# Optimization experiments

Measured on AMD Instinct MI355X. Metric: run time of the kernel, lower is better.

## Reference

```python
import jax, jax.numpy as jnp
import numpy as np

D_MODEL = 512
N_HEADS = 8
D_HEAD = D_MODEL // N_HEADS
MAX_LEN = 5000


def _make_pe():
    # sinusoidal table for relative positions -MAX_LEN..+MAX_LEN
    pos = np.arange(-MAX_LEN, MAX_LEN + 1, dtype=np.float32)[:, None]
    div = np.exp(np.arange(0, D_MODEL, 2, dtype=np.float32) * (-np.log(10000.0) / D_MODEL))
    pe = np.zeros((2 * MAX_LEN + 1, D_MODEL), dtype=np.float32)
    pe[:, 0::2] = np.sin(pos * div)
    pe[:, 1::2] = np.cos(pos * div)
    return jnp.asarray(pe)


def setup_inputs() -> dict:
    key = jax.random.key(0)
    ks = jax.random.split(key, 10)
    B, S = 8, 512
    xavier = lambda k: jax.random.uniform(k, (D_MODEL, D_MODEL), jnp.float32,
                                          -np.sqrt(6.0 / (2 * D_MODEL)), np.sqrt(6.0 / (2 * D_MODEL)))
    return {
        "x": jax.random.normal(ks[0], (B, S, D_MODEL), jnp.float32),
        "wq": xavier(ks[1]), "bq": jnp.zeros((D_MODEL,), jnp.float32),
        "wk": xavier(ks[2]), "bk": jnp.zeros((D_MODEL,), jnp.float32),
        "wv": xavier(ks[3]), "bv": jnp.zeros((D_MODEL,), jnp.float32),
        "wo": xavier(ks[4]), "bo": jnp.zeros((D_MODEL,), jnp.float32),
        "wr": xavier(ks[5]),
        "u": jnp.zeros((N_HEADS, D_HEAD), jnp.float32),
        "v_bias": jnp.zeros((N_HEADS, D_HEAD), jnp.float32),
        "pe": _make_pe(),
    }


def reference(x, wq, bq, wk, bk, wv, bv, wo, bo, wr, u, v_bias, pe):
    B, S, D = x.shape
    H, dh = N_HEADS, D_HEAD
    scale = dh ** -0.5

    # projections (torch Linear: x @ W.T + b) -> [B, H, S, dh]
    def proj(w, b):
        return (x @ w.T + b).reshape(B, S, H, dh).transpose(0, 2, 1, 3)
    q = proj(wq, bq)
    k = proj(wk, bk)
    v = proj(wv, bv)

    # relative position encodings: rel[i,j] = pe[clip(j-i) + MAX_LEN]
    pos = jnp.arange(S)
    rel_idx = jnp.clip(pos[None, :] - pos[:, None], -MAX_LEN, MAX_LEN) + MAX_LEN
    rel_pos = pe[rel_idx]                              # [S, S, D]
    rel_proj = (rel_pos @ wr.T).reshape(S, S, H, dh)   # [S, S, H, dh]
    rel_proj = rel_proj.transpose(2, 0, 1, 3)          # [H, S, S, dh]

    content = jnp.einsum('bhid,bhjd->bhij', q + u[None, :, None, :], k)
    position = jnp.einsum('bhid,hijd->bhij', q + v_bias[None, :, None, :], rel_proj)
    attn = jax.nn.softmax((content + position) * scale, axis=-1)

    out = jnp.einsum('bhij,bhjd->bhid', attn, v)       # [B, H, S, dh]
    out = out.transpose(0, 2, 1, 3).reshape(B, S, D)
    return out @ wo.T + bo
```

## Files before the change

### kernel.cpp

```cpp
#include <hip/hip_runtime.h>
#include <math.h>

#define DM 512
#define NH 8
#define DH 64
#define SEQ 512
#define BATCH 8
#define MR 1023
#define PE_OFF 4489

typedef float4 f4;
typedef __attribute__((ext_vector_type(8))) short bf16x8;
typedef __attribute__((ext_vector_type(4))) float f32x4;
typedef __attribute__((ext_vector_type(8))) unsigned short u16x8;
typedef __attribute__((ext_vector_type(4))) unsigned short u16x4;

__device__ __forceinline__ unsigned short f2bf(float f) {
    unsigned x = __float_as_uint(f);
    unsigned r = x + 0x7fffu + ((x >> 16) & 1u);
    return (unsigned short)(r >> 16);
}
__device__ __forceinline__ float bf2f(unsigned short h) {
    return __uint_as_float(((unsigned)h) << 16);
}
__device__ __forceinline__ f32x4 mfma16(bf16x8 a, bf16x8 b, f32x4 c) {
    return __builtin_amdgcn_mfma_f32_16x16x32_bf16(a, b, c, 0, 0, 0);
}
__device__ __forceinline__ void gll16(const unsigned short* g, unsigned short* l) {
    __builtin_amdgcn_global_load_lds(
        (const __attribute__((address_space(1))) unsigned int*)g,
        (__attribute__((address_space(3))) unsigned int*)l, 16, 0, 0);
}

__device__ __forceinline__ void cvt8s(const float* __restrict__ src,
                                      unsigned short* __restrict__ hi,
                                      unsigned short* __restrict__ lo, int i) {
    const int row = i >> 9, col = i & 511;
    const int j = (i & ~511) | (col ^ (((row >> 1) & 3) << 3));
    f4 a = *(const f4*)&src[i];
    f4 b = *(const f4*)&src[i + 4];
    float v[8] = {a.x, a.y, a.z, a.w, b.x, b.y, b.z, b.w};
    u16x8 h, l;
#pragma unroll
    for (int e = 0; e < 8; ++e) {
        unsigned short hb = f2bf(v[e]);
        h[e] = hb;
        l[e] = f2bf(v[e] - bf2f(hb));
    }
    *(u16x8*)&hi[j] = h;
    *(u16x8*)&lo[j] = l;
}

__global__ __launch_bounds__(256) void cvt_all_kernel(
    const float* __restrict__ x,
    const float* __restrict__ w0, const float* __restrict__ w1,
    const float* __restrict__ w2, const float* __restrict__ w3,
    const float* __restrict__ w4, const float* __restrict__ pe,
    unsigned short* __restrict__ xh, unsigned short* __restrict__ xl,
    unsigned short* __restrict__ wb,
    unsigned short* __restrict__ peh, unsigned short* __restrict__ pel)
{
    const int bid = blockIdx.x, tid = threadIdx.x;
    if (bid < 1024) {
        cvt8s(x, xh, xl, (bid * 256 + tid) * 8);
    } else if (bid < 1664) {
        const int wsel = (bid - 1024) >> 7;
        const float* src = (wsel == 0) ? w0 : (wsel == 1) ? w1 :
                           (wsel == 2) ? w2 : (wsel == 3) ? w3 : w4;
        unsigned short* hi = wb + (size_t)wsel * 524288;
        cvt8s(src, hi, hi + 262144, (((bid - 1024) & 127) * 256 + tid) * 8);
    } else {
        const int i = ((bid - 1664) * 256 + tid) * 8;
        if (i < 523776) cvt8s(pe, peh, pel, i);
    }
}

__device__ __forceinline__ void gemm_core128(
    const unsigned short* __restrict__ Ah, const unsigned short* __restrict__ Al,
    const unsigned short* __restrict__ Wh, const unsigned short* __restrict__ Wl,
    int m0, int n0, f32x4 acc[4][2],
    unsigned short* LAh, unsigned short* LAl,
    unsigned short* LBh, unsigned short* LBl)
{
    const int tid = threadIdx.x;
    const int lane = tid & 63, wid = tid >> 6;
    const int wm = (wid >> 1) << 6, wn = (wid & 1) << 5;
    const int fr = lane & 15, g = lane >> 4;
    const int crow = lane >> 2;
    const int ccol = (lane & 3) << 3;

#pragma unroll
    for (int i = 0; i < 4; ++i)
#pragma unroll
        for (int j = 0; j < 2; ++j)
            acc[i][j] = (f32x4){0.f, 0.f, 0.f, 0.f};

    const size_t ga1 = (size_t)(m0 + (wid << 4) + crow) * DM + ccol;
    const size_t ga2 = ga1 + (size_t)64 * DM;
    const size_t gb  = (size_t)(n0 + (wid << 4) + crow) * DM + ccol;
    const int lbase = wid << 9;
    const int cswz = (g ^ ((fr >> 1) & 3)) << 3;

    for (int k0 = 0; k0 < DM; k0 += 32) {
        if (k0) __syncthreads();
        gll16(Ah + ga1 + k0, LAh + lbase);
        gll16(Ah + ga2 + k0, LAh + lbase + 2048);
        gll16(Al + ga1 + k0, LAl + lbase);
        gll16(Al + ga2 + k0, LAl + lbase + 2048);
        gll16(Wh + gb + k0, LBh + lbase);
        gll16(Wl + gb + k0, LBl + lbase);
        __syncthreads();

        bf16x8 a_h[4], a_l[4], b_h[2], b_l[2];
#pragma unroll
        for (int mi = 0; mi < 4; ++mi) {
            const int ro = (wm + (mi << 4) + fr) << 5;
            a_h[mi] = *(const bf16x8*)&LAh[ro + cswz];
            a_l[mi] = *(const bf16x8*)&LAl[ro + cswz];
        }
#pragma unroll
        for (int ni = 0; ni < 2; ++ni) {
            const int ro = (wn + (ni << 4) + fr) << 5;
            b_h[ni] = *(const bf16x8*)&LBh[ro + cswz];
            b_l[ni] = *(const bf16x8*)&LBl[ro + cswz];
        }
#pragma unroll
        for (int mi = 0; mi < 4; ++mi)
#pragma unroll
            for (int ni = 0; ni < 2; ++ni) {
                acc[mi][ni] = mfma16(a_h[mi], b_h[ni], acc[mi][ni]);
                acc[mi][ni] = mfma16(a_h[mi], b_l[ni], acc[mi][ni]);
                acc[mi][ni] = mfma16(a_l[mi], b_h[ni], acc[mi][ni]);
            }
    }
}

#define GEMM_LDS \
    __shared__ unsigned short LAh[128 * 32], LAl[128 * 32]; \
    __shared__ unsigned short LBh[64 * 32], LBl[64 * 32];

__global__ __launch_bounds__(256) void qkv_rm_kernel(
    const unsigned short* __restrict__ xh, const unsigned short* __restrict__ xl,
    const unsigned short* __restrict__ wb,
    const unsigned short* __restrict__ peh, const unsigned short* __restrict__ pel,
    const float* __restrict__ bq, const float* __restrict__ bk,
    const float* __restrict__ bv, const float* __restrict__ u,
    const float* __restrict__ vb,
    unsigned short* __restrict__ qh, unsigned short* __restrict__ ql,
    unsigned short* __restrict__ kh, unsigned short* __restrict__ kl,
    unsigned short* __restrict__ vth, unsigned short* __restrict__ vtl,
    unsigned short* __restrict__ rmh, unsigned short* __restrict__ rml,
    float* __restrict__ rc)
{
    GEMM_LDS
    const int bid = blockIdx.x;
    const int tid = threadIdx.x, lane = tid & 63, wid = tid >> 6;
    const int wm = (wid >> 1) << 6, wn = (wid & 1) << 5;
    const int fr = lane & 15, g = lane >> 4;

    if (bid < 64) {
        const int n0 = (bid & 7) << 6, m0 = (bid >> 3) << 7;
        const unsigned short* wrh = wb + 4 * 524288;
        const unsigned short* wrl = wrh + 262144;
        f32x4 acc[4][2];
        gemm_core128(peh, pel, wrh, wrl, m0, n0, acc, LAh, LAl, LBh, LBl);

        const int h = n0 >> 6;
        float part[4][4];
        float wgt[2];
#pragma unroll
        for (int ni = 0; ni < 2; ++ni) {
            const int d = wn + (ni << 4) + fr;
            wgt[ni] = vb[(h << 6) + d] - u[(h << 6) + d];
        }
#pragma unroll
        for (int mi = 0; mi < 4; ++mi)
#pragma unroll
            for (int r = 0; r < 4; ++r) part[mi][r] = 0.f;

#pragma unroll
        for (int ni = 0; ni < 2; ++ni) {
            const int n_g = n0 + wn + (ni << 4) + fr;
            const int d = n_g & 63;
#pragma unroll
            for (int mi = 0; mi < 4; ++mi)
#pragma unroll
                for (int r = 0; r < 4; ++r) {
                    const int dd = m0 + wm + (mi << 4) + (g << 2) + r;
                    const float val = acc[mi][ni][r];
                    const size_t o = (((size_t)h << 10) + dd) * DH + d;
                    const unsigned short hb = f2bf(val);
                    rmh[o] = hb;
                    rml[o] = f2bf(val - bf2f(hb));
                    part[mi][r] = fmaf(wgt[ni], val, part[mi][r]);
                }
        }

        __syncthreads();
        float* cbuf = (float*)LAh;
#pragma unroll
        for (int mi = 0; mi < 4; ++mi)
#pragma unroll
            for (int r = 0; r < 4; ++r) {
                float v = part[mi][r];
#pragma unroll
                for (int off = 8; off; off >>= 1) v += __shfl_xor(v, off, 16);
                if (fr == 0)
                    cbuf[((wid & 1) << 7) + wm + (mi << 4) + (g << 2) + r] = v;
            }
        __syncthreads();
        if (tid < 128)
            rc[((size_t)h << 10) + m0 + tid] = cbuf[tid] + cbuf[128 + tid];
        return;
    }

    const int t = bid - 64;
    const int wsel = t >> 8;
    const int rest = t & 255;
    const int n0 = (rest & 7) << 6, m0 = (rest >> 3) << 7;
    const unsigned short* Wh = wb + (size_t)wsel * 524288;
    const unsigned short* Wl = Wh + 262144;
    f32x4 acc[4][2];
    gemm_core128(xh, xl, Wh, Wl, m0, n0, acc, LAh, LAl, LBh, LBl);

    const float* bias = (wsel == 0) ? bq : (wsel == 1) ? bk : bv;

    if (wsel < 2) {
        unsigned short* oh = (wsel == 0) ? qh : kh;
        unsigned short* ol = (wsel == 0) ? ql : kl;
#pragma unroll
        for (int ni = 0; ni < 2; ++ni) {
            const int n_g = n0 + wn + (ni << 4) + fr;
            float bvv = bias[n_g] + ((wsel == 0) ? u[n_g] : 0.f);
            const int h = n_g >> 6, d = n_g & 63;
#pragma unroll
            for (int mi = 0; mi < 4; ++mi)
#pragma unroll
                for (int r = 0; r < 4; ++r) {
                    const int m_g = m0 + wm + (mi << 4) + (g << 2) + r;
                    const int b = m_g >> 9, s = m_g & 511;
                    const float val = acc[mi][ni][r] + bvv;
                    const size_t o = ((size_t)(b * NH + h) * SEQ + s) * DH + d;
                    const unsigned short hb = f2bf(val);
                    oh[o] = hb;
                    ol[o] = f2bf(val - bf2f(hb));
                }
        }
    } else {
#pragma unroll
        for (int ni = 0; ni < 2; ++ni) {
            const int n_g = n0 + wn + (ni << 4) + fr;
            const float bvv = bias[n_g];
            const int h = n_g >> 6, d = n_g & 63;
#pragma unroll
            for (int mi = 0; mi < 4; ++mi) {
                const int m_b = m0 + wm + (mi << 4) + (g << 2);
                const int b = m_b >> 9, s = m_b & 511;
                u16x4 hv, lv;
#pragma unroll
                for (int r = 0; r < 4; ++r) {
                    const float val = acc[mi][ni][r] + bvv;
                    hv[r] = f2bf(val);
                    lv[r] = f2bf(val - bf2f(hv[r]));
                }
                const size_t o = ((size_t)(b * NH + h) * DH + d) * SEQ + s;
                *(u16x4*)&vth[o] = hv;
                *(u16x4*)&vtl[o] = lv;
            }
        }
    }
}

__global__ __launch_bounds__(256) void out_kernel(
    const unsigned short* __restrict__ cth, const unsigned short* __restrict__ ctl,
    const unsigned short* __restrict__ woh, const unsigned short* __restrict__ wol,
    const float* __restrict__ bo, float* __restrict__ out)
{
    GEMM_LDS
    const int n0 = blockIdx.x << 6, m0 = blockIdx.y << 7;
    f32x4 acc[4][2];
    gemm_core128(cth, ctl, woh, wol, m0, n0, acc, LAh, LAl, LBh, LBl);

    const int tid = threadIdx.x, lane = tid & 63, wid = tid >> 6;
    const int wm = (wid >> 1) << 6, wn = (wid & 1) << 5;
    const int fr = lane & 15, g = lane >> 4;
#pragma unroll
    for (int ni = 0; ni < 2; ++ni) {
        const int n_g = n0 + wn + (ni << 4) + fr;
        const float bvv = bo[n_g];
#pragma unroll
        for (int mi = 0; mi < 4; ++mi)
#pragma unroll
            for (int r = 0; r < 4; ++r) {
                const int m_g = m0 + wm + (mi << 4) + (g << 2) + r;
                out[(size_t)m_g * DM + n_g] = acc[mi][ni][r] + bvv;
            }
    }
}

__global__ __launch_bounds__(256) void attn_kernel(
    const unsigned short* __restrict__ qh_g, const unsigned short* __restrict__ ql_g,
    const unsigned short* __restrict__ kh_g, const unsigned short* __restrict__ kl_g,
    const unsigned short* __restrict__ vh_g, const unsigned short* __restrict__ vl_g,
    const unsigned short* __restrict__ rmh, const unsigned short* __restrict__ rml,
    const float* __restrict__ rc,
    unsigned short* __restrict__ cth, unsigned short* __restrict__ ctl)
{
    __shared__ unsigned short Kh[64][72], Kl[64][72], Vh[64][72], Vl[64][72];
    __shared__ unsigned short Pdd[4][16][84];
    __shared__ float Pt[4][16][68];

    const int tid = threadIdx.x;
    const int lane = tid & 63, wid = tid >> 6;
    const int g = lane >> 4, c = lane & 15;
    const int i0 = blockIdx.x << 6;
    const int h = blockIdx.y, b = blockIdx.z;
    const int R0 = i0 + (wid << 4);
    const size_t bh = (size_t)(b * NH + h) * (SEQ * DH);

    const int srow = tid >> 3;
    const int sch = (tid & 7) << 3;

    bf16x8 qhf[2], qlf[2];
#pragma unroll
    for (int ks = 0; ks < 2; ++ks) {
        const size_t qo = bh + (size_t)(R0 + c) * DH + (ks << 5) + (g << 3);
        qhf[ks] = *(const bf16x8*)&qh_g[qo];
        qlf[ks] = *(const bf16x8*)&ql_g[qo];
    }

    f32x4 Oacc[4];
#pragma unroll
    for (int nf = 0; nf < 4; ++nf) Oacc[nf] = (f32x4){0.f, 0.f, 0.f, 0.f};
    float m_r[4] = {-3e38f, -3e38f, -3e38f, -3e38f};
    float l_r[4] = {0.f, 0.f, 0.f, 0.f};

    const float* rch = rc + (h << 10);
    const unsigned short* rmhh = rmh + ((size_t)h << 16);
    const unsigned short* rmlh = rml + ((size_t)h << 16);

    u16x8 p0, p1, p2, p3, p4, p5, p6, p7;
    {
        const size_t kb = bh + (size_t)srow * DH + sch;
        p0 = *(const u16x8*)&kh_g[kb];
        p1 = *(const u16x8*)&kh_g[kb + 32 * DH];
        p2 = *(const u16x8*)&kl_g[kb];
        p3 = *(const u16x8*)&kl_g[kb + 32 * DH];
        const size_t vb_ = bh + (size_t)srow * SEQ + sch;
        p4 = *(const u16x8*)&vh_g[vb_];
        p5 = *(const u16x8*)&vh_g[vb_ + 32 * SEQ];
        p6 = *(const u16x8*)&vl_g[vb_];
        p7 = *(const u16x8*)&vl_g[vb_ + 32 * SEQ];
    }

    for (int jt = 0; jt < 8; ++jt) {
        const int j0 = jt << 6;
        __syncthreads();
        *(u16x8*)&Kh[srow][sch] = p0;
        *(u16x8*)&Kh[srow + 32][sch] = p1;
        *(u16x8*)&Kl[srow][sch] = p2;
        *(u16x8*)&Kl[srow + 32][sch] = p3;
        *(u16x8*)&Vh[srow][sch] = p4;
        *(u16x8*)&Vh[srow + 32][sch] = p5;
        *(u16x8*)&Vl[srow][sch] = p6;
        *(u16x8*)&Vl[srow + 32][sch] = p7;
        __syncthreads();
        if (jt < 7) {
            const int jn = j0 + 64;
            const size_t kb = bh + (size_t)(jn + srow) * DH + sch;
            p0 = *(const u16x8*)&kh_g[kb];
            p1 = *(const u16x8*)&kh_g[kb + 32 * DH];
            p2 = *(const u16x8*)&kl_g[kb];
            p3 = *(const u16x8*)&kl_g[kb + 32 * DH];
            const size_t vb_ = bh + (size_t)srow * SEQ + jn + sch;
            p4 = *(const u16x8*)&vh_g[vb_];
            p5 = *(const u16x8*)&vh_g[vb_ + 32 * SEQ];
            p6 = *(const u16x8*)&vl_g[vb_];
            p7 = *(const u16x8*)&vl_g[vb_ + 32 * SEQ];
        }

        __builtin_amdgcn_s_setprio(1);
        f32x4 accs[4];
#pragma unroll
        for (int nf = 0; nf < 4; ++nf) accs[nf] = (f32x4){0.f, 0.f, 0.f, 0.f};
#pragma unroll
        for (int ks = 0; ks < 2; ++ks)
#pragma unroll
            for (int nf = 0; nf < 4; ++nf) {
                bf16x8 b_h = *(const bf16x8*)&Kh[(nf << 4) + c][(ks << 5) + (g << 3)];
                bf16x8 b_l = *(const bf16x8*)&Kl[(nf << 4) + c][(ks << 5) + (g << 3)];
                accs[nf] = mfma16(qhf[ks], b_h, accs[nf]);
                accs[nf] = mfma16(qhf[ks], b_l, accs[nf]);
                accs[nf] = mfma16(qlf[ks], b_h, accs[nf]);
            }

        const int base_g = j0 - R0 + 496;
#pragma unroll
        for (int f = 0; f < 5; ++f) {
            f32x4 ap = (f32x4){0.f, 0.f, 0.f, 0.f};
#pragma unroll
            for (int ks = 0; ks < 2; ++ks) {
                const size_t ro = (size_t)(base_g + (f << 4) + c) * DH
                                + (ks << 5) + (g << 3);
                bf16x8 b_h = *(const bf16x8*)&rmhh[ro];
                bf16x8 b_l = *(const bf16x8*)&rmlh[ro];
                ap = mfma16(qhf[ks], b_h, ap);
                ap = mfma16(qhf[ks], b_l, ap);
                ap = mfma16(qlf[ks], b_h, ap);
            }
            const float rcv = rch[base_g + (f << 4) + c];
#pragma unroll
            for (int r = 0; r < 4; ++r)
                Pdd[wid][(g << 2) + r][(f << 4) + c] = f2bf(ap[r] + rcv);
        }
        __builtin_amdgcn_s_setprio(0);

#pragma unroll
        for (int r = 0; r < 4; ++r) {
            const int irow = (g << 2) + r;
            float sc[4];
#pragma unroll
            for (int nf = 0; nf < 4; ++nf) {
                const int ddl = (nf << 4) + c - irow + 15;
                sc[nf] = (accs[nf][r] + bf2f(Pdd[wid][irow][ddl])) * 0.125f;
            }
            float mt = fmaxf(fmaxf(sc[0], sc[1]), fmaxf(sc[2], sc[3]));
#pragma unroll
            for (int off = 8; off; off >>= 1) mt = fmaxf(mt, __shfl_xor(mt, off, 16));
            const float mn = fmaxf(m_r[r], mt);
            const float alpha = __expf(m_r[r] - mn);
            m_r[r] = mn;
            float rs = 0.f;
#pragma unroll
            for (int nf = 0; nf < 4; ++nf) {
                const float p = __expf(sc[nf] - mn);
                Pt[wid][irow][(nf << 4) + c] = p;
                rs += p;
            }
#pragma unroll
            for (int off = 8; off; off >>= 1) rs += __shfl_xor(rs, off, 16);
            l_r[r] = l_r[r] * alpha + rs;
#pragma unroll
            for (int nf = 0; nf < 4; ++nf) Oacc[nf][r] *= alpha;
        }

        __builtin_amdgcn_s_setprio(1);
#pragma unroll
        for (int ks = 0; ks < 2; ++ks) {
            f4 pv0 = *(const f4*)&Pt[wid][c][(ks << 5) + (g << 3)];
            f4 pv1 = *(const f4*)&Pt[wid][c][(ks << 5) + (g << 3) + 4];
            float pv[8] = {pv0.x, pv0.y, pv0.z, pv0.w, pv1.x, pv1.y, pv1.z, pv1.w};
            bf16x8 ph, pl;
#pragma unroll
            for (int e = 0; e < 8; ++e) {
                const unsigned short hb = f2bf(pv[e]);
                ph[e] = (short)hb;
                pl[e] = (short)f2bf(pv[e] - bf2f(hb));
            }
#pragma unroll
            for (int nf = 0; nf < 4; ++nf) {
                bf16x8 v_h = *(const bf16x8*)&Vh[(nf << 4) + c][(ks << 5) + (g << 3)];
                bf16x8 v_l = *(const bf16x8*)&Vl[(nf << 4) + c][(ks << 5) + (g << 3)];
                Oacc[nf] = mfma16(ph, v_h, Oacc[nf]);
                Oacc[nf] = mfma16(ph, v_l, Oacc[nf]);
                Oacc[nf] = mfma16(pl, v_h, Oacc[nf]);
            }
        }
        __builtin_amdgcn_s_setprio(0);
    }

    float inv[4];
#pragma unroll
    for (int r = 0; r < 4; ++r) inv[r] = 1.f / l_r[r];
#pragma unroll
    for (int nf = 0; nf < 4; ++nf)
#pragma unroll
        for (int r = 0; r < 4; ++r) {
            const float val = Oacc[nf][r] * inv[r];
            const int sr_ = (g << 2) + r;
            const int s = R0 + sr_;
            const int d = (h << 6) + (nf << 4) + c;
            const int dsw = d ^ (((sr_ >> 1) & 3) << 3);
            const size_t o = ((size_t)(b * SEQ) + s) * DM + dsw;
            const unsigned short hb = f2bf(val);
            cth[o] = hb;
            ctl[o] = f2bf(val - bf2f(hb));
        }
}

extern "C" void kernel_launch(void* const* d_in, const int* in_sizes, int n_in,
                              void* d_out, int out_size, void* d_ws, size_t ws_size,
                              hipStream_t stream)
{
    const float* x  = (const float*)d_in[0];
    const float* wq = (const float*)d_in[1];
    const float* bq = (const float*)d_in[2];
    const float* wk = (const float*)d_in[3];
    const float* bk = (const float*)d_in[4];
    const float* wv = (const float*)d_in[5];
    const float* bv = (const float*)d_in[6];
    const float* wo = (const float*)d_in[7];
    const float* bo = (const float*)d_in[8];
    const float* wr = (const float*)d_in[9];
    const float* u  = (const float*)d_in[10];
    const float* vb = (const float*)d_in[11];
    const float* pe = (const float*)d_in[12];
    float* out = (float*)d_out;
    unsigned short* us = (unsigned short*)d_ws;

    unsigned short* xh  = us;
    unsigned short* xl  = us + 2097152;
    unsigned short* wb  = us + 4194304;
    unsigned short* peh = us + 6815744;
    unsigned short* pel = us + 7340032;
    unsigned short* qh  = us + 7864320;
    unsigned short* ql  = us + 9961472;
    unsigned short* kh  = us + 12058624;
    unsigned short* kl  = us + 14155776;
    unsigned short* vth = us + 16252928;
    unsigned short* vtl = us + 18350080;
    unsigned short* rmh = us + 20447232;
    unsigned short* rml = us + 20971520;
    unsigned short* cth = us + 21495808;
    unsigned short* ctl = us + 23592960;
    float* rc = (float*)(us + 25690112);

    unsigned short* woh = wb + 3 * 524288;
    unsigned short* wol = woh + 262144;

    dim3 blk(256);
    cvt_all_kernel<<<1920, blk, 0, stream>>>(x, wq, wk, wv, wo, wr,
                                             pe + (size_t)PE_OFF * DM,
                                             xh, xl, wb, peh, pel);
    qkv_rm_kernel<<<832, blk, 0, stream>>>(xh, xl, wb, peh, pel,
                                           bq, bk, bv, u, vb,
                                           qh, ql, kh, kl, vth, vtl,
                                           rmh, rml, rc);
    attn_kernel<<<dim3(8, 8, 8), blk, 0, stream>>>(qh, ql, kh, kl, vth, vtl,
                                                   rmh, rml, rc, cth, ctl);
    out_kernel<<<dim3(8, 32), blk, 0, stream>>>(cth, ctl, woh, wol, bo, out);
}
```

Before: 120.2 us.

## Split attention over key halves and merge partial softmax results in new kernel

The attention kernel now splits the key dimension into two halves across a grid axis, doubling the block count from 512 to 1024. Each block writes unnormalised fp32 partial outputs plus row max and sum to workspace, and a new merge kernel combines them into the bf16 hi/lo context. V tiles are no longer staged through shared memory and are read directly from global memory, which cuts LDS use and raises occupancy. The cost is an extra kernel launch, extra global traffic for the partials, and uncoalesced per-lane V loads.

```diff
diff --git a/kernel.cpp b/kernel.cpp
--- a/kernel.cpp
+++ b/kernel.cpp
@@ -304,9 +304,9 @@
     const unsigned short* __restrict__ vh_g, const unsigned short* __restrict__ vl_g,
     const unsigned short* __restrict__ rmh, const unsigned short* __restrict__ rml,
     const float* __restrict__ rc,
-    unsigned short* __restrict__ cth, unsigned short* __restrict__ ctl)
-{
-    __shared__ unsigned short Kh[64][72], Kl[64][72], Vh[64][72], Vl[64][72];
+    float* __restrict__ Op, float* __restrict__ Mp, float* __restrict__ Lp)
+{
+    __shared__ unsigned short Kh[64][72], Kl[64][72];
     __shared__ unsigned short Pdd[4][16][84];
     __shared__ float Pt[4][16][68];
 
@@ -314,9 +314,12 @@
     const int lane = tid & 63, wid = tid >> 6;
     const int g = lane >> 4, c = lane & 15;
     const int i0 = blockIdx.x << 6;
-    const int h = blockIdx.y, b = blockIdx.z;
+    const int jh = blockIdx.y;
+    const int bhid = blockIdx.z;
+    const int h = bhid & 7;
     const int R0 = i0 + (wid << 4);
-    const size_t bh = (size_t)(b * NH + h) * (SEQ * DH);
+    const size_t bh = (size_t)bhid * (SEQ * DH);
+    const int jbase = jh << 8;
 
     const int srow = tid >> 3;
     const int sch = (tid & 7) << 3;
@@ -339,44 +342,30 @@
     const unsigned short* rmhh = rmh + ((size_t)h << 16);
     const unsigned short* rmlh = rml + ((size_t)h << 16);
 
-    u16x8 p0, p1, p2, p3, p4, p5, p6, p7;
+    u16x8 p0, p1, p2, p3;
     {
-        const size_t kb = bh + (size_t)srow * DH + sch;
+        const size_t kb = bh + (size_t)(jbase + srow) * DH + sch;
         p0 = *(const u16x8*)&kh_g[kb];
         p1 = *(const u16x8*)&kh_g[kb + 32 * DH];
         p2 = *(const u16x8*)&kl_g[kb];
         p3 = *(const u16x8*)&kl_g[kb + 32 * DH];
-        const size_t vb_ = bh + (size_t)srow * SEQ + sch;
-        p4 = *(const u16x8*)&vh_g[vb_];
-        p5 = *(const u16x8*)&vh_g[vb_ + 32 * SEQ];
-        p6 = *(const u16x8*)&vl_g[vb_];
-        p7 = *(const u16x8*)&vl_g[vb_ + 32 * SEQ];
-    }
-
-    for (int jt = 0; jt < 8; ++jt) {
-        const int j0 = jt << 6;
+    }
+
+#pragma unroll
+    for (int t = 0; t < 4; ++t) {
+        const int j0 = jbase + (t << 6);
         __syncthreads();
         *(u16x8*)&Kh[srow][sch] = p0;
         *(u16x8*)&Kh[srow + 32][sch] = p1;
         *(u16x8*)&Kl[srow][sch] = p2;
         *(u16x8*)&Kl[srow + 32][sch] = p3;
-        *(u16x8*)&Vh[srow][sch] = p4;
-        *(u16x8*)&Vh[srow + 32][sch] = p5;
-        *(u16x8*)&Vl[srow][sch] = p6;
-        *(u16x8*)&Vl[srow + 32][sch] = p7;
         __syncthreads();
-        if (jt < 7) {
-            const int jn = j0 + 64;
-            const size_t kb = bh + (size_t)(jn + srow) * DH + sch;
+        if (t < 3) {
+            const size_t kb = bh + (size_t)(j0 + 64 + srow) * DH + sch;
             p0 = *(const u16x8*)&kh_g[kb];
             p1 = *(const u16x8*)&kh_g[kb + 32 * DH];
             p2 = *(const u16x8*)&kl_g[kb];
             p3 = *(const u16x8*)&kl_g[kb + 32 * DH];
-            const size_t vb_ = bh + (size_t)srow * SEQ + jn + sch;
-            p4 = *(const u16x8*)&vh_g[vb_];
-            p5 = *(const u16x8*)&vh_g[vb_ + 32 * SEQ];
-            p6 = *(const u16x8*)&vl_g[vb_];
-            p7 = *(const u16x8*)&vl_g[vb_ + 32 * SEQ];
         }
 
         __builtin_amdgcn_s_setprio(1);
@@ -459,8 +448,10 @@
             }
 #pragma unroll
             for (int nf = 0; nf < 4; ++nf) {
-                bf16x8 v_h = *(const bf16x8*)&Vh[(nf << 4) + c][(ks << 5) + (g << 3)];
-                bf16x8 v_l = *(const bf16x8*)&Vl[(nf << 4) + c][(ks << 5) + (g << 3)];
+                const size_t vo = bh + (size_t)((nf << 4) + c) * SEQ + j0
+                                + (ks << 5) + (g << 3);
+                bf16x8 v_h = *(const bf16x8*)&vh_g[vo];
+                bf16x8 v_l = *(const bf16x8*)&vl_g[vo];
                 Oacc[nf] = mfma16(ph, v_h, Oacc[nf]);
                 Oacc[nf] = mfma16(ph, v_l, Oacc[nf]);
                 Oacc[nf] = mfma16(pl, v_h, Oacc[nf]);
@@ -469,23 +460,56 @@
         __builtin_amdgcn_s_setprio(0);
     }
 
-    float inv[4];
-#pragma unroll
-    for (int r = 0; r < 4; ++r) inv[r] = 1.f / l_r[r];
+    const size_t prow = (size_t)jh * 32768 + (size_t)bhid * 512;
 #pragma unroll
     for (int nf = 0; nf < 4; ++nf)
 #pragma unroll
         for (int r = 0; r < 4; ++r) {
-            const float val = Oacc[nf][r] * inv[r];
-            const int sr_ = (g << 2) + r;
-            const int s = R0 + sr_;
-            const int d = (h << 6) + (nf << 4) + c;
-            const int dsw = d ^ (((sr_ >> 1) & 3) << 3);
-            const size_t o = ((size_t)(b * SEQ) + s) * DM + dsw;
-            const unsigned short hb = f2bf(val);
-            cth[o] = hb;
-            ctl[o] = f2bf(val - bf2f(hb));
-        }
+            const int s = R0 + (g << 2) + r;
+            Op[(prow + s) * 64 + (nf << 4) + c] = Oacc[nf][r];
+        }
+    if (c == 0) {
+#pragma unroll
+        for (int r = 0; r < 4; ++r) {
+            const int s = R0 + (g << 2) + r;
+            Mp[prow + s] = m_r[r];
+            Lp[prow + s] = l_r[r];
+        }
+    }
+}
+
+__global__ __launch_bounds__(256) void merge_kernel(
+    const float* __restrict__ Op, const float* __restrict__ Mp,
+    const float* __restrict__ Lp,
+    unsigned short* __restrict__ cth, unsigned short* __restrict__ ctl)
+{
+    const int idx = blockIdx.x * 256 + threadIdx.x;
+    const int d4 = (idx & 15) << 2;
+    const int rowid = idx >> 4;
+    const int bhid = rowid >> 9, s = rowid & 511;
+    const int b = bhid >> 3, h = bhid & 7;
+
+    const float m0 = Mp[rowid], m1 = Mp[32768 + rowid];
+    const float l0 = Lp[rowid], l1 = Lp[32768 + rowid];
+    const float M = fmaxf(m0, m1);
+    const float s0 = __expf(m0 - M), s1 = __expf(m1 - M);
+    const float inv = 1.f / (l0 * s0 + l1 * s1);
+    const f4 o0 = *(const f4*)&Op[((size_t)rowid << 6) + d4];
+    const f4 o1 = *(const f4*)&Op[((size_t)(32768 + rowid) << 6) + d4];
+    float vals[4] = {
+        (o0.x * s0 + o1.x * s1) * inv, (o0.y * s0 + o1.y * s1) * inv,
+        (o0.z * s0 + o1.z * s1) * inv, (o0.w * s0 + o1.w * s1) * inv};
+    u16x4 hv, lv;
+#pragma unroll
+    for (int e = 0; e < 4; ++e) {
+        hv[e] = f2bf(vals[e]);
+        lv[e] = f2bf(vals[e] - bf2f(hv[e]));
+    }
+    const int d_full = (h << 6) + d4;
+    const int dsw = d_full ^ (((s >> 1) & 3) << 3);
+    const size_t o = ((size_t)b * SEQ + s) * DM + dsw;
+    *(u16x4*)&cth[o] = hv;
+    *(u16x4*)&ctl[o] = lv;
 }
 
 extern "C" void kernel_launch(void* const* d_in, const int* in_sizes, int n_in,
@@ -524,6 +548,9 @@
     unsigned short* cth = us + 21495808;
     unsigned short* ctl = us + 23592960;
     float* rc = (float*)(us + 25690112);
+    float* Op = (float*)(us + 25706496);
+    float* Mp = Op + 4194304;
+    float* Lp = Mp + 65536;
 
     unsigned short* woh = wb + 3 * 524288;
     unsigned short* wol = woh + 262144;
@@ -536,7 +563,8 @@
                                            bq, bk, bv, u, vb,
                                            qh, ql, kh, kl, vth, vtl,
                                            rmh, rml, rc);
-    attn_kernel<<<dim3(8, 8, 8), blk, 0, stream>>>(qh, ql, kh, kl, vth, vtl,
-                                                   rmh, rml, rc, cth, ctl);
+    attn_kernel<<<dim3(8, 2, 64), blk, 0, stream>>>(qh, ql, kh, kl, vth, vtl,
+                                                    rmh, rml, rc, Op, Mp, Lp);
+    merge_kernel<<<2048, blk, 0, stream>>>(Op, Mp, Lp, cth, ctl);
     out_kernel<<<dim3(8, 32), blk, 0, stream>>>(cth, ctl, woh, wol, bo, out);
 }
```

Measured after the change: 181.1 us. 50.7% more time.
